# Performance work log

Hardware: AMD Instinct MI355X
Metric: run time of the kernel (lower is better)

## Reference

```python
import jax, jax.numpy as jnp
import numpy as np

THETA = 10000.0
D_K = 128
MAX_SEQ_LEN = 16384
B, S = 8, 16384


def _make_tables(theta, d_k, max_seq_len):
    # thetas[p, i] = p / theta^(2i/d_k), matching the original einsum
    inv_freq = 1.0 / (theta ** (2.0 * jnp.arange(d_k // 2, dtype=jnp.float32) / d_k))
    ang = jnp.arange(max_seq_len, dtype=jnp.float32)[:, None] * inv_freq[None, :]
    return jnp.cos(ang), jnp.sin(ang)  # each (max_seq_len, d_k//2)


def setup_inputs() -> dict:
    key = jax.random.key(0)
    x = jax.random.normal(key, (B, S, D_K), dtype=jnp.float32)
    cos_tab, sin_tab = _make_tables(THETA, D_K, MAX_SEQ_LEN)
    token_positions = jnp.arange(S, dtype=jnp.int32)
    return {"x": x, "cos_tab": cos_tab, "sin_tab": sin_tab,
            "token_positions": token_positions}


def reference(x, cos_tab, sin_tab, token_positions):
    # Gather per-position rotation coefficients: (S, d_k//2)
    cos = cos_tab[token_positions]
    sin = sin_tab[token_positions]
    # The original's block-diag matrix rotates interleaved pairs (2i, 2i+1):
    # out_even = cos*x_even - sin*x_odd ; out_odd = sin*x_even + cos*x_odd
    x_even = x[..., 0::2]  # (B, S, d_k//2)
    x_odd = x[..., 1::2]
    out_even = cos * x_even - sin * x_odd
    out_odd = sin * x_even + cos * x_odd
    # interleave back to (B, S, d_k)
    return jnp.stack([out_even, out_odd], axis=-1).reshape(x.shape)
```

## Files before the change

kernel.cpp:

```cpp
#include <hip/hip_runtime.h>


typedef float f32x4 __attribute__((ext_vector_type(4)));
typedef float f32x2 __attribute__((ext_vector_type(2)));

#define S_LEN 16384
#define DK    128
#define NF4_PER_ROW (DK / 4)
#define N_F4  (8 * S_LEN * NF4_PER_ROW)
#define BLOCK 256
#define GRID  2048
#define STRIDE (GRID * BLOCK)
#define ITERS (N_F4 / STRIDE)

__global__ __launch_bounds__(BLOCK) void rope_f32_kernel(
    const f32x4* __restrict__ x,
    const f32x2* __restrict__ cos_tab,
    const f32x2* __restrict__ sin_tab,
    const int*   __restrict__ tok_pos,
    f32x4*       __restrict__ out)
{
    int t = blockIdx.x * BLOCK + threadIdx.x;
    const int j   = t & (NF4_PER_ROW - 1);
    const int s   = t >> 5;
    const int pos = tok_pos[s];

    const f32x2 c  = cos_tab[pos * (DK / 4) + j];
    const f32x2 sn = sin_tab[pos * (DK / 4) + j];

#pragma unroll 1
    for (int i = 0; i < ITERS; ++i, t += STRIDE) {
        const f32x4 v = x[t];
        f32x4 o;
        o.x = c.x * v.x - sn.x * v.y;
        o.y = sn.x * v.x + c.x * v.y;
        o.z = c.y * v.z - sn.y * v.w;
        o.w = sn.y * v.z + c.y * v.w;
        out[t] = o;
    }
}

extern "C" void kernel_launch(void* const* d_in, const int* in_sizes, int n_in,
                              void* d_out, int out_size, void* d_ws, size_t ws_size,
                              hipStream_t stream) {
    const f32x4* x   = (const f32x4*)d_in[0];
    const f32x2* ct  = (const f32x2*)d_in[1];
    const f32x2* st  = (const f32x2*)d_in[2];
    const int*   tp  = (const int*)d_in[3];
    f32x4*       out = (f32x4*)d_out;

    rope_f32_kernel<<<GRID, BLOCK, 0, stream>>>(x, ct, st, tp, out);
}
```

Measured before the change: 27.20 us.

## Replace grid-stride loop with one-shot grid processing two float4 per thread

Drops the persistent grid-stride loop, which reused cached cos/sin across batch iterations. The new version launches enough blocks to cover the whole tensor, with each thread handling two float4 elements. Each thread now re-gathers its own token position and cos/sin pair, and both loads are issued up front to increase memory-level parallelism. The cost is more total table reads and many more blocks.

```diff
diff --git a/kernel.cpp b/kernel.cpp
--- a/kernel.cpp
+++ b/kernel.cpp
@@ -7,11 +7,7 @@
 #define S_LEN 16384
 #define DK    128
 #define NF4_PER_ROW (DK / 4)
-#define N_F4  (8 * S_LEN * NF4_PER_ROW)
 #define BLOCK 256
-#define GRID  2048
-#define STRIDE (GRID * BLOCK)
-#define ITERS (N_F4 / STRIDE)
 
 __global__ __launch_bounds__(BLOCK) void rope_f32_kernel(
     const f32x4* __restrict__ x,
@@ -20,24 +16,37 @@
     const int*   __restrict__ tok_pos,
     f32x4*       __restrict__ out)
 {
-    int t = blockIdx.x * BLOCK + threadIdx.x;
-    const int j   = t & (NF4_PER_ROW - 1);
-    const int s   = t >> 5;
-    const int pos = tok_pos[s];
+    const int t0 = blockIdx.x * (2 * BLOCK) + threadIdx.x;
+    const int t1 = t0 + BLOCK;
 
-    const f32x2 c  = cos_tab[pos * (DK / 4) + j];
-    const f32x2 sn = sin_tab[pos * (DK / 4) + j];
+    const int j0 = t0 & (NF4_PER_ROW - 1);
+    const int s0 = (t0 >> 5) & (S_LEN - 1);
+    const int j1 = t1 & (NF4_PER_ROW - 1);
+    const int s1 = (t1 >> 5) & (S_LEN - 1);
 
-#pragma unroll 1
-    for (int i = 0; i < ITERS; ++i, t += STRIDE) {
-        const f32x4 v = x[t];
-        f32x4 o;
-        o.x = c.x * v.x - sn.x * v.y;
-        o.y = sn.x * v.x + c.x * v.y;
-        o.z = c.y * v.z - sn.y * v.w;
-        o.w = sn.y * v.z + c.y * v.w;
-        out[t] = o;
-    }
+    const int pos0 = tok_pos[s0];
+    const int pos1 = tok_pos[s1];
+
+    const f32x4 v0 = x[t0];
+    const f32x4 v1 = x[t1];
+    const f32x2 c0  = cos_tab[pos0 * (DK / 4) + j0];
+    const f32x2 sn0 = sin_tab[pos0 * (DK / 4) + j0];
+    const f32x2 c1  = cos_tab[pos1 * (DK / 4) + j1];
+    const f32x2 sn1 = sin_tab[pos1 * (DK / 4) + j1];
+
+    f32x4 o0, o1;
+    o0.x = c0.x * v0.x - sn0.x * v0.y;
+    o0.y = sn0.x * v0.x + c0.x * v0.y;
+    o0.z = c0.y * v0.z - sn0.y * v0.w;
+    o0.w = sn0.y * v0.z + c0.y * v0.w;
+
+    o1.x = c1.x * v1.x - sn1.x * v1.y;
+    o1.y = sn1.x * v1.x + c1.x * v1.y;
+    o1.z = c1.y * v1.z - sn1.y * v1.w;
+    o1.w = sn1.y * v1.z + c1.y * v1.w;
+
+    out[t0] = o0;
+    out[t1] = o1;
 }
 
 extern "C" void kernel_launch(void* const* d_in, const int* in_sizes, int n_in,
@@ -49,5 +58,8 @@
     const int*   tp  = (const int*)d_in[3];
     f32x4*       out = (f32x4*)d_out;
 
-    rope_f32_kernel<<<GRID, BLOCK, 0, stream>>>(x, ct, st, tp, out);
+    const int n_f4  = out_size / 4;
+    const int grid  = n_f4 / (2 * BLOCK);
+
+    rope_f32_kernel<<<grid, BLOCK, 0, stream>>>(x, ct, st, tp, out);
 }
```

Result: faster. 25.33 us (median of 2 runs) (-6.9%).

## Replace grid-stride loop with unrolled per-thread batching of loads

Applied to the files above, without the earlier changes.

Drops the grid-stride loop, which loaded the cos/sin coefficients once per thread and reused them across all batches. Each thread now handles four consecutive float4 chunks, issuing all x loads up front and then gathering cos/sin per chunk. The launch grid is derived from the output size. The aim is more memory requests in flight per thread, at the cost of re-reading the rotation tables once per batch instead of once overall.

```diff
diff --git a/kernel.cpp b/kernel.cpp
--- a/kernel.cpp
+++ b/kernel.cpp
@@ -7,11 +7,8 @@
 #define S_LEN 16384
 #define DK    128
 #define NF4_PER_ROW (DK / 4)
-#define N_F4  (8 * S_LEN * NF4_PER_ROW)
 #define BLOCK 256
-#define GRID  2048
-#define STRIDE (GRID * BLOCK)
-#define ITERS (N_F4 / STRIDE)
+#define UNROLL 4
 
 __global__ __launch_bounds__(BLOCK) void rope_f32_kernel(
     const f32x4* __restrict__ x,
@@ -20,23 +17,33 @@
     const int*   __restrict__ tok_pos,
     f32x4*       __restrict__ out)
 {
-    int t = blockIdx.x * BLOCK + threadIdx.x;
-    const int j   = t & (NF4_PER_ROW - 1);
-    const int s   = t >> 5;
-    const int pos = tok_pos[s];
+    const int base = blockIdx.x * (UNROLL * BLOCK) + threadIdx.x;
 
-    const f32x2 c  = cos_tab[pos * (DK / 4) + j];
-    const f32x2 sn = sin_tab[pos * (DK / 4) + j];
+    int   t[UNROLL];
+    f32x4 v[UNROLL];
+    f32x2 c[UNROLL], sn[UNROLL];
 
-#pragma unroll 1
-    for (int i = 0; i < ITERS; ++i, t += STRIDE) {
-        const f32x4 v = x[t];
+#pragma unroll
+    for (int u = 0; u < UNROLL; ++u) {
+        t[u] = base + u * BLOCK;
+        v[u] = x[t[u]];
+    }
+#pragma unroll
+    for (int u = 0; u < UNROLL; ++u) {
+        const int j   = t[u] & (NF4_PER_ROW - 1);
+        const int s   = (t[u] >> 5) & (S_LEN - 1);
+        const int pos = tok_pos[s];
+        c[u]  = cos_tab[pos * (DK / 4) + j];
+        sn[u] = sin_tab[pos * (DK / 4) + j];
+    }
+#pragma unroll
+    for (int u = 0; u < UNROLL; ++u) {
         f32x4 o;
-        o.x = c.x * v.x - sn.x * v.y;
-        o.y = sn.x * v.x + c.x * v.y;
-        o.z = c.y * v.z - sn.y * v.w;
-        o.w = sn.y * v.z + c.y * v.w;
-        out[t] = o;
+        o.x = c[u].x * v[u].x - sn[u].x * v[u].y;
+        o.y = sn[u].x * v[u].x + c[u].x * v[u].y;
+        o.z = c[u].y * v[u].z - sn[u].y * v[u].w;
+        o.w = sn[u].y * v[u].z + c[u].y * v[u].w;
+        out[t[u]] = o;
     }
 }
 
@@ -49,5 +56,8 @@
     const int*   tp  = (const int*)d_in[3];
     f32x4*       out = (f32x4*)d_out;
 
-    rope_f32_kernel<<<GRID, BLOCK, 0, stream>>>(x, ct, st, tp, out);
+    const int n_f4  = out_size / 4;
+    const int grid  = n_f4 / (UNROLL * BLOCK);
+
+    rope_f32_kernel<<<grid, BLOCK, 0, stream>>>(x, ct, st, tp, out);
 }
```

Measured after the change: 25.82 us. 5.1% less time.
